# Performance work log

Measured on AMD Instinct MI355X. Metric: run time of the kernel, lower is better.

The kernel has to match this reference:

```python
import jax, jax.numpy as jnp
import numpy as np

NUM_IDS = 64  # static upper bound on track ids (0 = background)


def setup_inputs() -> dict:
    key = jax.random.key(0)
    k1, k2 = jax.random.split(key)
    B, F, C, H, W = 4, 8, 16, 256, 256
    embeddings = jax.random.normal(k1, (B, F, C, H, W), dtype=jnp.float32)
    track_ids = jax.random.randint(k2, (B, F, 1, H, W), 0, NUM_IDS, dtype=jnp.int32)
    return {"embeddings": embeddings, "track_ids": track_ids}


def reference(embeddings, track_ids):
    B, F, C, H, W = embeddings.shape
    K = NUM_IDS
    ids = track_ids[:, :, 0]  # (B, F, H, W)
    # global segment id: one bucket per (b, f, track_id)
    seg = ((jnp.arange(B * F, dtype=jnp.int32).reshape(B, F, 1, 1)) * K + ids).reshape(-1)
    data = jnp.transpose(embeddings, (0, 1, 3, 4, 2)).reshape(-1, C)  # (B*F*H*W, C)
    sums = jax.ops.segment_sum(data, seg, num_segments=B * F * K).reshape(B, F, K, C)
    counts = jax.ops.segment_sum(jnp.ones((B * F * H * W,), embeddings.dtype), seg,
                                 num_segments=B * F * K).reshape(B, F, K)
    means = sums / jnp.maximum(counts, 1)[..., None]  # (B, F, K, C)
    present = counts > 0
    # id must be > 0 (background excluded) and present in both consecutive frames
    pair_valid = present[:, :-1] & present[:, 1:] & (jnp.arange(K) > 0)  # (B, F-1, K)
    dist = jnp.sum((means[:, :-1] - means[:, 1:]) ** 2, axis=-1)  # (B, F-1, K)
    total = jnp.sum(jnp.where(pair_valid, dist, jnp.zeros_like(dist)))
    n_valid = jnp.sum(pair_valid).astype(embeddings.dtype)
    return jnp.where(n_valid > 0, total / n_valid, jnp.zeros_like(total))
```

## Files before the change

kernel.cpp:

```cpp
#include <hip/hip_runtime.h>
#include <hip/hip_bf16.h>

#define NB 4
#define NF 8
#define NC 16
#define NK 64
#define HW 65536
#define NBF 32
#define BPF 64
#define PPB (HW / BPF)
#define PPW (PPB / 4)
#define STEPS (PPW / 32)
#define PARTSZ 1088

typedef __attribute__((ext_vector_type(8))) short bf16x8;
typedef __attribute__((ext_vector_type(4))) float f32x4;

__device__ __forceinline__ short f32_to_bf16_bits(float x) {
    union { float f; unsigned u; } v; v.f = x;
    unsigned r = v.u + 0x7FFFu + ((v.u >> 16) & 1u);
    return (short)(r >> 16);
}

__global__ __launch_bounds__(256) void accum_mfma(const float* __restrict__ E,
                                                  const int* __restrict__ T,
                                                  float* __restrict__ part) {
    __shared__ int   sids[PPB];
    __shared__ float lsum[4][NK][NC];
    __shared__ float lcnt[4][NK];

    const int tid = threadIdx.x;
    const int wv  = tid >> 6;
    const int l   = tid & 63;
    const int col = l & 15;
    const int grp = l >> 4;

    const int bf    = blockIdx.x / BPF;
    const int chunk = blockIdx.x % BPF;

    *reinterpret_cast<int4*>(&sids[tid * 4]) =
        *reinterpret_cast<const int4*>(T + (size_t)bf * HW + chunk * PPB + tid * 4);

    const int base = chunk * PPB + wv * PPW + grp * 8;
    const float* Ep = E + ((size_t)bf * NC + col) * HW + base;
    const int* sip = &sids[wv * PPW + grp * 8];

    float4 dbuf[2 * STEPS];
    #pragma unroll
    for (int s = 0; s < STEPS; ++s) {
        dbuf[2 * s]     = *reinterpret_cast<const float4*>(Ep + s * 32);
        dbuf[2 * s + 1] = *reinterpret_cast<const float4*>(Ep + s * 32 + 4);
    }

    __syncthreads();

    f32x4 accS[4], accC[4];
    #pragma unroll
    for (int t = 0; t < 4; ++t) { accS[t] = (f32x4){0,0,0,0}; accC[t] = (f32x4){0,0,0,0}; }

    bf16x8 bOnes;
    {
        const short ov = (col == 0) ? (short)0x3F80 : (short)0;
        #pragma unroll
        for (int j = 0; j < 8; ++j) bOnes[j] = ov;
    }

    #pragma unroll
    for (int s = 0; s < STEPS; ++s) {
        const int off = s * 32;
        const int4 i0 = *reinterpret_cast<const int4*>(sip + off);
        const int4 i1 = *reinterpret_cast<const int4*>(sip + off + 4);
        const float4 d0 = dbuf[2 * s];
        const float4 d1 = dbuf[2 * s + 1];

        const int   idv[8] = {i0.x, i0.y, i0.z, i0.w, i1.x, i1.y, i1.z, i1.w};
        const float dv[8]  = {d0.x, d0.y, d0.z, d0.w, d1.x, d1.y, d1.z, d1.w};

        bf16x8 bF;
        #pragma unroll
        for (int j = 0; j < 8; ++j) bF[j] = f32_to_bf16_bits(dv[j]);

        #pragma unroll
        for (int t = 0; t < 4; ++t) {
            const int ktar = t * 16 + col;
            bf16x8 aT;
            #pragma unroll
            for (int j = 0; j < 8; ++j) aT[j] = (idv[j] == ktar) ? (short)0x3F80 : (short)0;
            accS[t] = __builtin_amdgcn_mfma_f32_16x16x32_bf16(aT, bF,    accS[t], 0, 0, 0);
            accC[t] = __builtin_amdgcn_mfma_f32_16x16x32_bf16(aT, bOnes, accC[t], 0, 0, 0);
        }
    }

    #pragma unroll
    for (int t = 0; t < 4; ++t) {
        #pragma unroll
        for (int j = 0; j < 4; ++j) {
            const int k = t * 16 + grp * 4 + j;
            lsum[wv][k][col] = accS[t][j];
            if (col == 0) lcnt[wv][k] = accC[t][j];
        }
    }
    __syncthreads();

    float* pp = part + (size_t)blockIdx.x * PARTSZ;
    const float* lp = &lsum[0][0][0];
    for (int i = tid; i < NK * NC; i += 256) {
        pp[i] = lp[i] + lp[NK*NC + i] + lp[2*NK*NC + i] + lp[3*NK*NC + i];
    }
    if (tid < NK) {
        pp[NK * NC + tid] = lcnt[0][tid] + lcnt[1][tid] + lcnt[2][tid] + lcnt[3][tid];
    }
}

__global__ __launch_bounds__(256) void reduce_kernel(const float* __restrict__ part,
                                                     float* __restrict__ gsum,
                                                     float* __restrict__ gcnt) {
    const int e = blockIdx.x * 256 + threadIdx.x;
    if (e < NBF * NK * NC) {
        const int bf = e >> 10;
        const int i  = e & 1023;
        const float* p = part + (size_t)(bf * BPF) * PARTSZ + i;
        float s = 0.0f;
        #pragma unroll 8
        for (int blk = 0; blk < BPF; ++blk) s += p[(size_t)blk * PARTSZ];
        gsum[e] = s;
    } else {
        const int e2 = e - NBF * NK * NC;
        const int bf = e2 >> 6;
        const int k  = e2 & 63;
        const float* p = part + (size_t)(bf * BPF) * PARTSZ + NK * NC + k;
        float s = 0.0f;
        #pragma unroll 8
        for (int blk = 0; blk < BPF; ++blk) s += p[(size_t)blk * PARTSZ];
        gcnt[e2] = s;
    }
}

__global__ __launch_bounds__(256) void finish_kernel(const float* __restrict__ gsum,
                                                     const float* __restrict__ gcnt,
                                                     float* __restrict__ out) {
    float total = 0.0f, nv = 0.0f;
    for (int idx = threadIdx.x; idx < NB * (NF - 1) * NK; idx += 256) {
        const int k = idx & 63;
        const int bfr = idx >> 6;
        const int b = bfr / (NF - 1);
        const int f = bfr % (NF - 1);
        const int bf0 = b * NF + f;
        if (k == 0) continue;
        const float c0 = gcnt[bf0 * NK + k];
        const float c1 = gcnt[(bf0 + 1) * NK + k];
        if (c0 > 0.0f && c1 > 0.0f) {
            const float r0 = 1.0f / c0, r1 = 1.0f / c1;
            float d = 0.0f;
            #pragma unroll
            for (int c = 0; c < NC; ++c) {
                const float m0 = gsum[(size_t)bf0 * (NK * NC) + k * NC + c] * r0;
                const float m1 = gsum[(size_t)(bf0 + 1) * (NK * NC) + k * NC + c] * r1;
                const float df = m0 - m1;
                d += df * df;
            }
            total += d;
            nv += 1.0f;
        }
    }
    const int lane = threadIdx.x & 63;
    const int wvi  = threadIdx.x >> 6;
    #pragma unroll
    for (int off = 32; off > 0; off >>= 1) {
        total += __shfl_down(total, off, 64);
        nv    += __shfl_down(nv, off, 64);
    }
    __shared__ float sT[4], sN[4];
    if (lane == 0) { sT[wvi] = total; sN[wvi] = nv; }
    __syncthreads();
    if (threadIdx.x == 0) {
        const float t = sT[0] + sT[1] + sT[2] + sT[3];
        const float n = sN[0] + sN[1] + sN[2] + sN[3];
        out[0] = (n > 0.0f) ? (t / n) : 0.0f;
    }
}

extern "C" void kernel_launch(void* const* d_in, const int* in_sizes, int n_in,
                              void* d_out, int out_size, void* d_ws, size_t ws_size,
                              hipStream_t stream) {
    const float* E = (const float*)d_in[0];
    const int*   T = (const int*)d_in[1];
    float* out = (float*)d_out;

    float* part = (float*)d_ws;
    float* gsum = part + (size_t)(NBF * BPF) * PARTSZ;
    float* gcnt = gsum + NBF * NK * NC;

    accum_mfma<<<NBF * BPF, 256, 0, stream>>>(E, T, part);
    reduce_kernel<<<(NBF * NK * NC + NBF * NK) / 256, 256, 0, stream>>>(part, gsum, gcnt);
    finish_kernel<<<1, 256, 0, stream>>>(gsum, gcnt, out);
}
```

Before: 207.5 us.

## Coalesce embedding loads and stage bf16 tiles in shared memory for MFMA

Each thread now reads one contiguous float4 per channel plane, so a block's global loads are fully coalesced. Previously each lane pulled 32-byte pieces from scattered channel planes. The values are converted to bf16 and written into a per-wave, padded LDS tile, and each lane reads back its MFMA B-fragment from there. The LDS tile is reused for the per-wave partial sums after a barrier. This cuts live registers and the load inefficiency, at the cost of extra LDS traffic and a larger shared-memory footprint.

```diff
diff --git a/kernel.cpp b/kernel.cpp
--- a/kernel.cpp
+++ b/kernel.cpp
@@ -12,21 +12,20 @@
 #define PPW (PPB / 4)
 #define STEPS (PPW / 32)
 #define PARTSZ 1088
+#define LTS 65
 
 typedef __attribute__((ext_vector_type(8))) short bf16x8;
 typedef __attribute__((ext_vector_type(4))) float f32x4;
 
-__device__ __forceinline__ short f32_to_bf16_bits(float x) {
-    union { float f; unsigned u; } v; v.f = x;
-    unsigned r = v.u + 0x7FFFu + ((v.u >> 16) & 1u);
-    return (short)(r >> 16);
+__device__ __forceinline__ unsigned bf16_rne(unsigned u) {
+    return u + 0x7FFFu + ((u >> 16) & 1u);
 }
 
 __global__ __launch_bounds__(256) void accum_mfma(const float* __restrict__ E,
                                                   const int* __restrict__ T,
                                                   float* __restrict__ part) {
+    __shared__ uint2 ltile[4][NC * LTS];
     __shared__ int   sids[PPB];
-    __shared__ float lsum[4][NK][NC];
     __shared__ float lcnt[4][NK];
 
     const int tid = threadIdx.x;
@@ -37,22 +36,28 @@
 
     const int bf    = blockIdx.x / BPF;
     const int chunk = blockIdx.x % BPF;
+    const size_t fbase = (size_t)bf * NC * HW + (size_t)chunk * PPB;
 
     *reinterpret_cast<int4*>(&sids[tid * 4]) =
         *reinterpret_cast<const int4*>(T + (size_t)bf * HW + chunk * PPB + tid * 4);
 
-    const int base = chunk * PPB + wv * PPW + grp * 8;
-    const float* Ep = E + ((size_t)bf * NC + col) * HW + base;
-    const int* sip = &sids[wv * PPW + grp * 8];
-
-    float4 dbuf[2 * STEPS];
-    #pragma unroll
-    for (int s = 0; s < STEPS; ++s) {
-        dbuf[2 * s]     = *reinterpret_cast<const float4*>(Ep + s * 32);
-        dbuf[2 * s + 1] = *reinterpret_cast<const float4*>(Ep + s * 32 + 4);
-    }
-
-    __syncthreads();
+    #pragma unroll 1
+    for (int b2 = 0; b2 < 2; ++b2) {
+        float4 dbuf[8];
+        #pragma unroll
+        for (int j = 0; j < 8; ++j)
+            dbuf[j] = *reinterpret_cast<const float4*>(
+                E + fbase + (size_t)(b2 * 8 + j) * HW + tid * 4);
+        #pragma unroll
+        for (int j = 0; j < 8; ++j) {
+            union { float f[4]; unsigned u[4]; } q;
+            q.f[0] = dbuf[j].x; q.f[1] = dbuf[j].y; q.f[2] = dbuf[j].z; q.f[3] = dbuf[j].w;
+            uint2 pk;
+            pk.x = (bf16_rne(q.u[0]) >> 16) | (bf16_rne(q.u[1]) & 0xFFFF0000u);
+            pk.y = (bf16_rne(q.u[2]) >> 16) | (bf16_rne(q.u[3]) & 0xFFFF0000u);
+            ltile[wv][(b2 * 8 + j) * LTS + l] = pk;
+        }
+    }
 
     f32x4 accS[4], accC[4];
     #pragma unroll
@@ -65,47 +70,45 @@
         for (int j = 0; j < 8; ++j) bOnes[j] = ov;
     }
 
+    const int*   sip = &sids[wv * PPW + grp * 8];
+    const uint2* bp  = &ltile[wv][col * LTS + grp * 2];
+
     #pragma unroll
     for (int s = 0; s < STEPS; ++s) {
-        const int off = s * 32;
-        const int4 i0 = *reinterpret_cast<const int4*>(sip + off);
-        const int4 i1 = *reinterpret_cast<const int4*>(sip + off + 4);
-        const float4 d0 = dbuf[2 * s];
-        const float4 d1 = dbuf[2 * s + 1];
-
-        const int   idv[8] = {i0.x, i0.y, i0.z, i0.w, i1.x, i1.y, i1.z, i1.w};
-        const float dv[8]  = {d0.x, d0.y, d0.z, d0.w, d1.x, d1.y, d1.z, d1.w};
-
-        bf16x8 bF;
-        #pragma unroll
-        for (int j = 0; j < 8; ++j) bF[j] = f32_to_bf16_bits(dv[j]);
-
+        const int4 i0 = *reinterpret_cast<const int4*>(sip + s * 32);
+        const int4 i1 = *reinterpret_cast<const int4*>(sip + s * 32 + 4);
+        union { bf16x8 v; uint2 u2[2]; } bu;
+        bu.u2[0] = bp[s * 8];
+        bu.u2[1] = bp[s * 8 + 1];
+
+        const int idv[8] = {i0.x, i0.y, i0.z, i0.w, i1.x, i1.y, i1.z, i1.w};
         #pragma unroll
         for (int t = 0; t < 4; ++t) {
             const int ktar = t * 16 + col;
             bf16x8 aT;
             #pragma unroll
             for (int j = 0; j < 8; ++j) aT[j] = (idv[j] == ktar) ? (short)0x3F80 : (short)0;
-            accS[t] = __builtin_amdgcn_mfma_f32_16x16x32_bf16(aT, bF,    accS[t], 0, 0, 0);
+            accS[t] = __builtin_amdgcn_mfma_f32_16x16x32_bf16(aT, bu.v,  accS[t], 0, 0, 0);
             accC[t] = __builtin_amdgcn_mfma_f32_16x16x32_bf16(aT, bOnes, accC[t], 0, 0, 0);
         }
     }
 
+    __syncthreads();
+    float* lsum = reinterpret_cast<float*>(&ltile[0][0]);
     #pragma unroll
     for (int t = 0; t < 4; ++t) {
         #pragma unroll
         for (int j = 0; j < 4; ++j) {
             const int k = t * 16 + grp * 4 + j;
-            lsum[wv][k][col] = accS[t][j];
+            lsum[((wv * NK) + k) * NC + col] = accS[t][j];
             if (col == 0) lcnt[wv][k] = accC[t][j];
         }
     }
     __syncthreads();
 
     float* pp = part + (size_t)blockIdx.x * PARTSZ;
-    const float* lp = &lsum[0][0][0];
     for (int i = tid; i < NK * NC; i += 256) {
-        pp[i] = lp[i] + lp[NK*NC + i] + lp[2*NK*NC + i] + lp[3*NK*NC + i];
+        pp[i] = lsum[i] + lsum[NK*NC + i] + lsum[2*NK*NC + i] + lsum[3*NK*NC + i];
     }
     if (tid < NK) {
         pp[NK * NC + tid] = lcnt[0][tid] + lcnt[1][tid] + lcnt[2][tid] + lcnt[3][tid];
```

Result: no change. 210.5 us (+1.5%).
